# Optimization experiments

Measured on AMD Instinct MI355X. Metric: run time of the kernel, lower is better.

## Reference

```python
import jax, jax.numpy as jnp
import numpy as np


def setup_inputs() -> dict:
    key = jax.random.key(0)
    k1, k2 = jax.random.split(key)
    B, N, M, D = 8, 8192, 8192, 3
    preds = jax.random.normal(k1, (B, M, D), dtype=jnp.float32)
    gts = jax.random.normal(k2, (B, N, D), dtype=jnp.float32)
    return {"preds": preds, "gts": gts}


def reference(preds, gts):
    # Faithful to torch: P = batch_pairwise_dist(x=gts, y=preds), shape [B, N_gts, N_preds]
    x = gts.astype(jnp.float32)
    y = preds.astype(jnp.float32)
    xx = jnp.sum(x * x, axis=-1)                      # [B, N]
    yy = jnp.sum(y * y, axis=-1)                      # [B, M]
    zz = jnp.einsum('bnd,bmd->bnm', x, y)             # [B, N, M]
    P = xx[:, :, None] + yy[:, None, :] - 2.0 * zz    # squared distances
    loss_1 = jnp.mean(jnp.min(P, axis=1))             # min over gts points
    loss_2 = jnp.mean(jnp.min(P, axis=2))             # min over pred points
    return loss_1 + loss_2
```

## Files before the change

kernel.cpp:

```cpp
#include <hip/hip_runtime.h>
#include <hip/hip_bf16.h>


typedef _Float16 f16x8 __attribute__((ext_vector_type(8)));
typedef float f32x16 __attribute__((ext_vector_type(16)));

#define NPTS 8192
#define BATCH 8
#define TPB 256
#define BN 256
#define BM 1024
#define NCHUNK (NPTS / BM)
#define CTPC (BM / 32)

__device__ __forceinline__ void cvt_split(float v, _Float16& h, _Float16& l) {
    h = (_Float16)v;
    l = (_Float16)(v - (float)h);
}

__global__ __launch_bounds__(TPB, 2) void chamfer_mfma_kernel(
    const float* __restrict__ preds, const float* __restrict__ gts,
    float* __restrict__ rowmin )
{
    __shared__ f16x8 ldsB[CTPC][2][32];

    const int bid  = blockIdx.x;
    const int pass = bid >> 8;
    const int rem  = bid & 255;
    const int b      = rem >> 5;
    const int rowblk = rem & 31;

    const float* __restrict__ Asrc = (pass == 0) ? gts : preds;
    const float* __restrict__ Bsrc = (pass == 0) ? preds : gts;
    const float* __restrict__ Ab = Asrc + (size_t)b * NPTS * 3;
    const float* __restrict__ Bb = Bsrc + (size_t)b * NPTS * 3;

    const int tid  = threadIdx.x;
    const int lane = tid & 63;
    const int w    = tid >> 6;
    const int kh   = lane >> 5;
    const int cl   = lane & 31;

    f16x8 af[2];
#pragma unroll
    for (int t = 0; t < 2; ++t) {
        const int row = rowblk * BN + w * 64 + t * 32 + cl;
        const float* xp = Ab + (size_t)row * 3;
        const float x0 = xp[0], x1 = xp[1], x2 = xp[2];
        _Float16 h0, l0, h1, l1, h2, l2;
        cvt_split(x0, h0, l0); cvt_split(x1, h1, l1); cvt_split(x2, h2, l2);
        const float xx = x0 * x0 + x1 * x1 + x2 * x2;
        _Float16 xxh, xxl; cvt_split(xx, xxh, xxl);
        const f16x8 lo = { h0, h1, h2, l0, l1, l2, h0, h1 };
        const f16x8 hi = { h2, (_Float16)1, (_Float16)1, xxh, xxl,
                           (_Float16)0, (_Float16)0, (_Float16)0 };
        af[t] = kh ? hi : lo;
    }

    const f16x8* __restrict__ bptr = &ldsB[0][kh][cl];
    const f32x16 zc = {};

    float rb[2][16];
#pragma unroll
    for (int t = 0; t < 2; ++t)
#pragma unroll
        for (int r = 0; r < 16; ++r) rb[t][r] = 1e30f;

    for (int chunk = 0; chunk < NCHUNK; ++chunk) {
        __syncthreads();
#pragma unroll
        for (int i = 0; i < BM / TPB; ++i) {
            const int pl = i * TPB + tid;
            const float* yp = Bb + (size_t)(chunk * BM + pl) * 3;
            const float y0 = yp[0], y1 = yp[1], y2 = yp[2];
            _Float16 nh0, nl0, nh1, nl1, nh2, nl2;
            { const float hf = (float)(_Float16)y0; nh0 = (_Float16)(-2.f * hf); nl0 = (_Float16)(-2.f * (y0 - hf)); }
            { const float hf = (float)(_Float16)y1; nh1 = (_Float16)(-2.f * hf); nl1 = (_Float16)(-2.f * (y1 - hf)); }
            { const float hf = (float)(_Float16)y2; nh2 = (_Float16)(-2.f * hf); nl2 = (_Float16)(-2.f * (y2 - hf)); }
            const float yy = y0 * y0 + y1 * y1 + y2 * y2;
            _Float16 yyh, yyl; cvt_split(yy, yyh, yyl);
            const f16x8 lo = { nh0, nh1, nh2, nh0, nh1, nh2, nl0, nl1 };
            const f16x8 hi = { nl2, yyh, yyl, (_Float16)1, (_Float16)1,
                               (_Float16)0, (_Float16)0, (_Float16)0 };
            ldsB[pl >> 5][0][pl & 31] = lo;
            ldsB[pl >> 5][1][pl & 31] = hi;
        }
        __syncthreads();

#pragma unroll 4
        for (int ct = 0; ct < CTPC; ++ct) {
            const f16x8 bf = bptr[ct * 64];
            const f32x16 a0 = __builtin_amdgcn_mfma_f32_32x32x16_f16(af[0], bf, zc, 0, 0, 0);
            const f32x16 a1 = __builtin_amdgcn_mfma_f32_32x32x16_f16(af[1], bf, zc, 0, 0, 0);
#pragma unroll
            for (int r = 0; r < 16; ++r) rb[0][r] = fminf(rb[0][r], a0[r]);
#pragma unroll
            for (int r = 0; r < 16; ++r) rb[1][r] = fminf(rb[1][r], a1[r]);
        }
    }

#pragma unroll
    for (int t = 0; t < 2; ++t)
#pragma unroll
        for (int r = 0; r < 16; ++r) {
            float v = rb[t][r];
            v = fminf(v, __shfl_xor(v, 1, 64));
            v = fminf(v, __shfl_xor(v, 2, 64));
            v = fminf(v, __shfl_xor(v, 4, 64));
            v = fminf(v, __shfl_xor(v, 8, 64));
            v = fminf(v, __shfl_xor(v, 16, 64));
            rb[t][r] = v;
        }

    if (cl == 0) {
        float* rbase = rowmin + ((size_t)(pass * BATCH + b) * NPTS)
                     + rowblk * BN + w * 64;
#pragma unroll
        for (int t = 0; t < 2; ++t)
#pragma unroll
            for (int r = 0; r < 16; ++r) {
                const int rloc = (r & 3) + 8 * (r >> 2) + 4 * kh;
                rbase[t * 32 + rloc] = rb[t][r];
            }
    }
}

__global__ __launch_bounds__(256) void chamfer_reduce1(
    const float* __restrict__ rowmin, float* __restrict__ bsums)
{
    const int gid = blockIdx.x * 256 + threadIdx.x;
    float m = rowmin[gid];
#pragma unroll
    for (int off = 32; off > 0; off >>= 1) m += __shfl_down(m, off, 64);

    __shared__ float wsum[4];
    const int lane = threadIdx.x & 63;
    const int wid  = threadIdx.x >> 6;
    if (lane == 0) wsum[wid] = m;
    __syncthreads();
    if (threadIdx.x == 0)
        bsums[blockIdx.x] = (wsum[0] + wsum[1]) + (wsum[2] + wsum[3]);
}

__global__ __launch_bounds__(512) void chamfer_reduce2(
    const float* __restrict__ bsums, float* __restrict__ out)
{
    float m = bsums[threadIdx.x];
#pragma unroll
    for (int off = 32; off > 0; off >>= 1) m += __shfl_down(m, off, 64);

    __shared__ float wsum[8];
    const int lane = threadIdx.x & 63;
    const int wid  = threadIdx.x >> 6;
    if (lane == 0) wsum[wid] = m;
    __syncthreads();
    if (threadIdx.x == 0) {
        float t = ((wsum[0] + wsum[1]) + (wsum[2] + wsum[3]))
                + ((wsum[4] + wsum[5]) + (wsum[6] + wsum[7]));
        out[0] = t * (1.0f / 65536.0f);
    }
}

extern "C" void kernel_launch(void* const* d_in, const int* in_sizes, int n_in,
                              void* d_out, int out_size, void* d_ws, size_t ws_size,
                              hipStream_t stream) {
    const float* preds = (const float*)d_in[0];
    const float* gts   = (const float*)d_in[1];
    float* out = (float*)d_out;

    float* rowmin = (float*)d_ws;
    float* bsums  = (float*)((char*)d_ws + (size_t)2 * BATCH * NPTS * sizeof(float));

    chamfer_mfma_kernel<<<512, TPB, 0, stream>>>(preds, gts, rowmin);
    chamfer_reduce1<<<512, 256, 0, stream>>>(rowmin, bsums);
    chamfer_reduce2<<<1, 512, 0, stream>>>(bsums, out);
}
```

Baseline: 47.77 us.

## Split column range across two blocks with larger row tiles and paired MFMA min

Each block now covers 512 query rows with 512 threads but only half of the reference columns; the two column halves write partial row minima that the first reduction kernel combines with a float2 min. The inner loop issues two MFMAs per B fragment pair and folds them with a nested fmin, shortening the min dependency chain. The goal is to halve the B-operand staging work per row and raise the occupancy target. The cost is double the partial writes and a tighter register budget under launch bounds (512,4).

```diff
diff --git a/kernel.cpp b/kernel.cpp
--- a/kernel.cpp
+++ b/kernel.cpp
@@ -7,28 +7,29 @@
 
 #define NPTS 8192
 #define BATCH 8
-#define TPB 256
-#define BN 256
+#define TPB 512
+#define BN 512
 #define BM 1024
-#define NCHUNK (NPTS / BM)
+#define CPB 4
 #define CTPC (BM / 32)
+#define NQ_TOT (2 * BATCH * NPTS)
 
 __device__ __forceinline__ void cvt_split(float v, _Float16& h, _Float16& l) {
     h = (_Float16)v;
     l = (_Float16)(v - (float)h);
 }
 
-__global__ __launch_bounds__(TPB, 2) void chamfer_mfma_kernel(
+__global__ __launch_bounds__(TPB, 4) void chamfer_mfma_kernel(
     const float* __restrict__ preds, const float* __restrict__ gts,
-    float* __restrict__ rowmin )
+    float* __restrict__ partial )
 {
     __shared__ f16x8 ldsB[CTPC][2][32];
 
     const int bid  = blockIdx.x;
     const int pass = bid >> 8;
-    const int rem  = bid & 255;
-    const int b      = rem >> 5;
-    const int rowblk = rem & 31;
+    const int b       = (bid >> 5) & 7;
+    const int rowblk  = (bid >> 1) & 15;
+    const int colhalf = bid & 1;
 
     const float* __restrict__ Asrc = (pass == 0) ? gts : preds;
     const float* __restrict__ Bsrc = (pass == 0) ? preds : gts;
@@ -66,12 +67,13 @@
 #pragma unroll
         for (int r = 0; r < 16; ++r) rb[t][r] = 1e30f;
 
-    for (int chunk = 0; chunk < NCHUNK; ++chunk) {
+    for (int chunk = 0; chunk < CPB; ++chunk) {
+        const int cbase = (colhalf * CPB + chunk) * BM;
         __syncthreads();
 #pragma unroll
         for (int i = 0; i < BM / TPB; ++i) {
             const int pl = i * TPB + tid;
-            const float* yp = Bb + (size_t)(chunk * BM + pl) * 3;
+            const float* yp = Bb + (size_t)(cbase + pl) * 3;
             const float y0 = yp[0], y1 = yp[1], y2 = yp[2];
             _Float16 nh0, nl0, nh1, nl1, nh2, nl2;
             { const float hf = (float)(_Float16)y0; nh0 = (_Float16)(-2.f * hf); nl0 = (_Float16)(-2.f * (y0 - hf)); }
@@ -87,15 +89,18 @@
         }
         __syncthreads();
 
-#pragma unroll 4
-        for (int ct = 0; ct < CTPC; ++ct) {
-            const f16x8 bf = bptr[ct * 64];
-            const f32x16 a0 = __builtin_amdgcn_mfma_f32_32x32x16_f16(af[0], bf, zc, 0, 0, 0);
-            const f32x16 a1 = __builtin_amdgcn_mfma_f32_32x32x16_f16(af[1], bf, zc, 0, 0, 0);
+#pragma unroll 2
+        for (int ct = 0; ct < CTPC; ct += 2) {
+            const f16x8 bfA = bptr[ct * 64];
+            const f16x8 bfB = bptr[(ct + 1) * 64];
 #pragma unroll
-            for (int r = 0; r < 16; ++r) rb[0][r] = fminf(rb[0][r], a0[r]);
+            for (int t = 0; t < 2; ++t) {
+                const f32x16 aA = __builtin_amdgcn_mfma_f32_32x32x16_f16(af[t], bfA, zc, 0, 0, 0);
+                const f32x16 aB = __builtin_amdgcn_mfma_f32_32x32x16_f16(af[t], bfB, zc, 0, 0, 0);
 #pragma unroll
-            for (int r = 0; r < 16; ++r) rb[1][r] = fminf(rb[1][r], a1[r]);
+                for (int r = 0; r < 16; ++r)
+                    rb[t][r] = fminf(fminf(aA[r], aB[r]), rb[t][r]);
+            }
         }
     }
 
@@ -113,23 +118,25 @@
         }
 
     if (cl == 0) {
-        float* rbase = rowmin + ((size_t)(pass * BATCH + b) * NPTS)
-                     + rowblk * BN + w * 64;
+        float* rbase = partial + (((size_t)(pass * BATCH + b) * NPTS)
+                     + rowblk * BN + w * 64) * 2 + colhalf;
 #pragma unroll
         for (int t = 0; t < 2; ++t)
 #pragma unroll
             for (int r = 0; r < 16; ++r) {
                 const int rloc = (r & 3) + 8 * (r >> 2) + 4 * kh;
-                rbase[t * 32 + rloc] = rb[t][r];
+                rbase[(t * 32 + rloc) * 2] = rb[t][r];
             }
     }
 }
 
 __global__ __launch_bounds__(256) void chamfer_reduce1(
-    const float* __restrict__ rowmin, float* __restrict__ bsums)
+    const float* __restrict__ partial, float* __restrict__ bsums)
 {
     const int gid = blockIdx.x * 256 + threadIdx.x;
-    float m = rowmin[gid];
+    const float2 v = ((const float2*)partial)[gid];
+    float m = fminf(v.x, v.y);
+
 #pragma unroll
     for (int off = 32; off > 0; off >>= 1) m += __shfl_down(m, off, 64);
 
@@ -168,10 +175,10 @@
     const float* gts   = (const float*)d_in[1];
     float* out = (float*)d_out;
 
-    float* rowmin = (float*)d_ws;
-    float* bsums  = (float*)((char*)d_ws + (size_t)2 * BATCH * NPTS * sizeof(float));
+    float* partial = (float*)d_ws;
+    float* bsums   = (float*)((char*)d_ws + (size_t)NQ_TOT * 2 * sizeof(float));
 
-    chamfer_mfma_kernel<<<512, TPB, 0, stream>>>(preds, gts, rowmin);
-    chamfer_reduce1<<<512, 256, 0, stream>>>(rowmin, bsums);
+    chamfer_mfma_kernel<<<512, TPB, 0, stream>>>(preds, gts, partial);
+    chamfer_reduce1<<<512, 256, 0, stream>>>(partial, bsums);
     chamfer_reduce2<<<1, 512, 0, stream>>>(bsums, out);
 }
```

After: 45.83 us. 1.04x faster.

## Double-buffer LDS point tiles and prefetch next chunk during MFMA loop

Applied to the files above, without the earlier changes.

The staged tile is halved to 512 points and two LDS buffers are used. The next chunk's global loads are issued before the MFMA/min loop and converted into the other buffer afterwards, so only one barrier per chunk remains. The inner loop also pairs two B tiles so their mins are merged before being folded into the running minimum. This aims to hide global load latency and cut barrier stalls, at the cost of more chunk iterations and extra registers for the prefetched values.

```diff
diff --git a/kernel.cpp b/kernel.cpp
--- a/kernel.cpp
+++ b/kernel.cpp
@@ -9,26 +9,25 @@
 #define BATCH 8
 #define TPB 256
 #define BN 256
-#define BM 1024
-#define NCHUNK (NPTS / BM)
-#define CTPC (BM / 32)
+#define CHUNK 512
+#define NCH (NPTS / CHUNK)
+#define CTPC (CHUNK / 32)
+#define NQ_TOT (2 * BATCH * NPTS)
 
 __device__ __forceinline__ void cvt_split(float v, _Float16& h, _Float16& l) {
-    h = (_Float16)v;
-    l = (_Float16)(v - (float)h);
+    h = (_Float16)v; l = (_Float16)(v - (float)h);
 }
 
 __global__ __launch_bounds__(TPB, 2) void chamfer_mfma_kernel(
     const float* __restrict__ preds, const float* __restrict__ gts,
     float* __restrict__ rowmin )
 {
-    __shared__ f16x8 ldsB[CTPC][2][32];
+    __shared__ f16x8 ldsB[2][CTPC][2][32];
 
     const int bid  = blockIdx.x;
     const int pass = bid >> 8;
-    const int rem  = bid & 255;
-    const int b      = rem >> 5;
-    const int rowblk = rem & 31;
+    const int b      = (bid >> 5) & 7;
+    const int rowblk = bid & 31;
 
     const float* __restrict__ Asrc = (pass == 0) ? gts : preds;
     const float* __restrict__ Bsrc = (pass == 0) ? preds : gts;
@@ -57,22 +56,21 @@
         af[t] = kh ? hi : lo;
     }
 
-    const f16x8* __restrict__ bptr = &ldsB[0][kh][cl];
     const f32x16 zc = {};
-
     float rb[2][16];
 #pragma unroll
     for (int t = 0; t < 2; ++t)
 #pragma unroll
         for (int r = 0; r < 16; ++r) rb[t][r] = 1e30f;
 
-    for (int chunk = 0; chunk < NCHUNK; ++chunk) {
-        __syncthreads();
+    auto stage = [&](int buf, float y00, float y01, float y02,
+                     float y10, float y11, float y12) {
 #pragma unroll
-        for (int i = 0; i < BM / TPB; ++i) {
+        for (int i = 0; i < 2; ++i) {
+            const float y0 = i ? y10 : y00;
+            const float y1 = i ? y11 : y01;
+            const float y2 = i ? y12 : y02;
             const int pl = i * TPB + tid;
-            const float* yp = Bb + (size_t)(chunk * BM + pl) * 3;
-            const float y0 = yp[0], y1 = yp[1], y2 = yp[2];
             _Float16 nh0, nl0, nh1, nl1, nh2, nl2;
             { const float hf = (float)(_Float16)y0; nh0 = (_Float16)(-2.f * hf); nl0 = (_Float16)(-2.f * (y0 - hf)); }
             { const float hf = (float)(_Float16)y1; nh1 = (_Float16)(-2.f * hf); nl1 = (_Float16)(-2.f * (y1 - hf)); }
@@ -82,21 +80,44 @@
             const f16x8 lo = { nh0, nh1, nh2, nh0, nh1, nh2, nl0, nl1 };
             const f16x8 hi = { nl2, yyh, yyl, (_Float16)1, (_Float16)1,
                                (_Float16)0, (_Float16)0, (_Float16)0 };
-            ldsB[pl >> 5][0][pl & 31] = lo;
-            ldsB[pl >> 5][1][pl & 31] = hi;
+            ldsB[buf][pl >> 5][0][pl & 31] = lo;
+            ldsB[buf][pl >> 5][1][pl & 31] = hi;
         }
+    };
+
+    {
+        const float* yp0 = Bb + (size_t)tid * 3;
+        const float* yp1 = yp0 + (size_t)TPB * 3;
+        stage(0, yp0[0], yp0[1], yp0[2], yp1[0], yp1[1], yp1[2]);
+    }
+    __syncthreads();
+
+    for (int c = 0; c < NCH; ++c) {
+        float g0 = 0.f, g1 = 0.f, g2 = 0.f, g3 = 0.f, g4 = 0.f, g5 = 0.f;
+        if (c + 1 < NCH) {
+            const float* yp0 = Bb + (size_t)((c + 1) * CHUNK + tid) * 3;
+            const float* yp1 = yp0 + (size_t)TPB * 3;
+            g0 = yp0[0]; g1 = yp0[1]; g2 = yp0[2];
+            g3 = yp1[0]; g4 = yp1[1]; g5 = yp1[2];
+        }
+
+        const f16x8* __restrict__ bptr = &ldsB[c & 1][0][kh][cl];
+#pragma unroll 2
+        for (int ct = 0; ct < CTPC; ct += 2) {
+            const f16x8 bfA = bptr[ct * 64];
+            const f16x8 bfB = bptr[(ct + 1) * 64];
+#pragma unroll
+            for (int t = 0; t < 2; ++t) {
+                const f32x16 aA = __builtin_amdgcn_mfma_f32_32x32x16_f16(af[t], bfA, zc, 0, 0, 0);
+                const f32x16 aB = __builtin_amdgcn_mfma_f32_32x32x16_f16(af[t], bfB, zc, 0, 0, 0);
+#pragma unroll
+                for (int r = 0; r < 16; ++r)
+                    rb[t][r] = fminf(fminf(aA[r], aB[r]), rb[t][r]);
+            }
+        }
+
+        if (c + 1 < NCH) stage((c + 1) & 1, g0, g1, g2, g3, g4, g5);
         __syncthreads();
-
-#pragma unroll 4
-        for (int ct = 0; ct < CTPC; ++ct) {
-            const f16x8 bf = bptr[ct * 64];
-            const f32x16 a0 = __builtin_amdgcn_mfma_f32_32x32x16_f16(af[0], bf, zc, 0, 0, 0);
-            const f32x16 a1 = __builtin_amdgcn_mfma_f32_32x32x16_f16(af[1], bf, zc, 0, 0, 0);
-#pragma unroll
-            for (int r = 0; r < 16; ++r) rb[0][r] = fminf(rb[0][r], a0[r]);
-#pragma unroll
-            for (int r = 0; r < 16; ++r) rb[1][r] = fminf(rb[1][r], a1[r]);
-        }
     }
 
 #pragma unroll
@@ -113,7 +134,7 @@
         }
 
     if (cl == 0) {
-        float* rbase = rowmin + ((size_t)(pass * BATCH + b) * NPTS)
+        float* rbase = rowmin + (size_t)(pass * BATCH + b) * NPTS
                      + rowblk * BN + w * 64;
 #pragma unroll
         for (int t = 0; t < 2; ++t)
@@ -169,7 +190,7 @@
     float* out = (float*)d_out;
 
     float* rowmin = (float*)d_ws;
-    float* bsums  = (float*)((char*)d_ws + (size_t)2 * BATCH * NPTS * sizeof(float));
+    float* bsums  = (float*)((char*)d_ws + (size_t)NQ_TOT * sizeof(float));
 
     chamfer_mfma_kernel<<<512, TPB, 0, stream>>>(preds, gts, rowmin);
     chamfer_reduce1<<<512, 256, 0, stream>>>(rowmin, bsums);
```

After: 48.52 us. Within noise of the previous version (+1.6%).
